# Kernel optimization log

Measured on AMD Instinct MI355X. Metric: run time of the kernel, lower is better.

The kernel has to match this reference:

```python
import jax, jax.numpy as jnp
import numpy as np
import itertools

N = 65536          # points
R = 1.0 / 16.0     # radius (forward uses 1/16)
K = 64             # max_num_neighbors in forward call
G = 16             # grid cells per axis (cell size == R)


def _radius_knn_edges(pts):
    """Grid-hashed radius search; per point keep nearest K within R (self-loop included),
    pad with self index so every point has exactly K edges (max-aggregation neutral)."""
    cells = np.minimum((pts / R).astype(np.int64), G - 1)
    cid = (cells[:, 0] * G + cells[:, 1]) * G + cells[:, 2]
    order = np.argsort(cid, kind='stable')
    sorted_cid = cid[order]
    counts = np.bincount(cid, minlength=G ** 3)
    starts = np.concatenate([[0], np.cumsum(counts)[:-1]])
    M = int(counts.max())
    cand = -np.ones((G ** 3, M), dtype=np.int64)
    slot = np.arange(N) - starts[sorted_cid]
    cand[sorted_cid, slot] = order
    offs = np.array(list(itertools.product([-1, 0, 1], repeat=3)))
    nbr = np.empty((N, K), dtype=np.int64)
    chunk = 4096
    for s in range(0, N, chunk):
        e = min(s + chunk, N)
        c = cells[s:e]
        nc = c[:, None, :] + offs[None]                      # [B,27,3]
        valid_c = np.all((nc >= 0) & (nc < G), axis=-1)      # [B,27]
        ncid = (nc[..., 0] * G + nc[..., 1]) * G + nc[..., 2]
        ncid = np.where(valid_c, ncid, 0)
        cd = cand[ncid]                                      # [B,27,M]
        cd = np.where(np.broadcast_to(valid_c[..., None], cd.shape), cd, -1)
        cd = cd.reshape(e - s, -1)                           # [B,27M]
        p = pts[np.maximum(cd, 0)]
        d = np.linalg.norm(p - pts[s:e, None, :], axis=-1)
        d = np.where((cd >= 0) & (d <= R), d, np.inf)
        sel = np.argsort(d, axis=1)[:, :K]
        row = np.arange(e - s)[:, None]
        picked = cd[row, sel]
        ok = np.isfinite(d[row, sel])
        nbr[s:e] = np.where(ok, picked, np.arange(s, e)[:, None])
    out_index = np.repeat(np.arange(N, dtype=np.int64), K)
    in_index = nbr.reshape(-1)
    return out_index, in_index


def setup_inputs() -> dict:
    key = jax.random.key(0)
    ks = jax.random.split(key, 16)
    pos = jax.random.uniform(ks[0], (N, 3), dtype=jnp.float32)
    rgb = jax.random.uniform(ks[1], (N, 3), dtype=jnp.float32)
    batch = jnp.zeros((N,), dtype=jnp.int64)
    oi, ii = _radius_knn_edges(np.asarray(pos, dtype=np.float64))
    out_index = jnp.asarray(oi)
    in_index = jnp.asarray(ii)

    def lin_w(k, fi, fo):
        return jax.random.normal(k, (fi, fo), dtype=jnp.float32) / np.sqrt(fi).astype(np.float32)

    def lin_b(k, fo):
        return 0.01 * jax.random.normal(k, (fo,), dtype=jnp.float32)

    return {
        'pos': pos, 'rgb': rgb, 'batch': batch,
        'out_index': out_index, 'in_index': in_index,
        'w1a': lin_w(ks[2], 6, 8),   'b1a': lin_b(ks[3], 8),
        'w1b': lin_w(ks[4], 8, 8),   'b1b': lin_b(ks[5], 8),
        'w2a': lin_w(ks[6], 11, 16), 'b2a': lin_b(ks[7], 16),
        'w2b': lin_w(ks[8], 16, 16), 'b2b': lin_b(ks[9], 16),
        'w3a': lin_w(ks[10], 19, 32), 'b3a': lin_b(ks[11], 32),
        'w3b': lin_w(ks[12], 32, 32), 'b3b': lin_b(ks[13], 32),
    }


def _point_conv(x, pos, out_index, in_index, wa, ba, wb, bb):
    # gather neighbor features + relative position, local MLP, max-scatter, output linear
    dpos = pos[in_index] - pos[out_index]                      # [E,3]
    msg = jnp.concatenate([x[in_index], dpos], axis=-1)        # [E,c_in+3]
    h = jax.nn.celu(msg @ wa + ba)                             # [E,c_mid]
    agg = jax.ops.segment_max(h, out_index, num_segments=pos.shape[0],
                              indices_are_sorted=True)         # [N,c_mid]
    return agg @ wb + bb                                       # [N,c_out]


def reference(pos, rgb, batch, out_index, in_index,
              w1a, b1a, w1b, b1b, w2a, b2a, w2b, b2b, w3a, b3a, w3b, b3b):
    out = jax.nn.celu(_point_conv(pos, pos, out_index, in_index, w1a, b1a, w1b, b1b))
    out = jax.nn.celu(_point_conv(out, pos, out_index, in_index, w2a, b2a, w2b, b2b))
    out = jax.nn.celu(_point_conv(out, pos, out_index, in_index, w3a, b3a, w3b, b3b))
    return (pos, out, batch)
```

## Files before the change

### kernel.cpp

```cpp
#include <hip/hip_runtime.h>
#include <hip/hip_fp16.h>
#include <math.h>


#define NPTS 65536
#define KNBR 64

__device__ __forceinline__ float celu1(float x) {
    return x > 0.0f ? x : (__expf(x) - 1.0f);
}

__device__ __forceinline__ unsigned pkmax(unsigned a, unsigned b) {
    unsigned d;
    asm("v_pk_max_f16 %0, %1, %2" : "=v"(d) : "v"(a), "v"(b));
    return d;
}

__device__ __forceinline__ unsigned pack2(float a, float b) {
    __half2 h = __floats2half2_rn(a, b);
    return *(unsigned*)&h;
}

__global__ __launch_bounds__(256) void k_prep1(
    const float* __restrict__ pos,
    const float* __restrict__ w1a,
    const float* __restrict__ b1a,
    __half* __restrict__ q1,
    float* __restrict__ dout,
    int out_size)
{
    int t = blockIdx.x * 256 + threadIdx.x;
    if (t >= NPTS) return;
    float p0 = pos[3 * t + 0];
    float p1 = pos[3 * t + 1];
    float p2 = pos[3 * t + 2];
    dout[3 * t + 0] = p0;
    dout[3 * t + 1] = p1;
    dout[3 * t + 2] = p2;
    float q[8];
#pragma unroll
    for (int c = 0; c < 8; ++c) {
        float a = b1a[c];
        a = fmaf(p0, w1a[0 * 8 + c] + w1a[3 * 8 + c], a);
        a = fmaf(p1, w1a[1 * 8 + c] + w1a[4 * 8 + c], a);
        a = fmaf(p2, w1a[2 * 8 + c] + w1a[5 * 8 + c], a);
        q[c] = a;
    }
    uint4 pk;
    pk.x = pack2(q[0], q[1]);
    pk.y = pack2(q[2], q[3]);
    pk.z = pack2(q[4], q[5]);
    pk.w = pack2(q[6], q[7]);
    *(uint4*)(q1 + 8 * t) = pk;
    for (int j = 35 * NPTS + t; j < out_size; j += NPTS)
        dout[j] = 0.0f;
}

template <int FH>
__global__ __launch_bounds__(256) void k_edge(
    const __half* __restrict__ q,
    const int* __restrict__ idx,
    __half* __restrict__ m)
{
    constexpr int SL  = FH / 8;
    constexpr int EG  = 16 / SL;
    constexpr int EPG = 64 / EG;

    int wave = (blockIdx.x * 256 + threadIdx.x) >> 6;
    int l  = threadIdx.x & 63;
    int pl = l >> 4;
    int u  = l & 15;
    int c  = u % SL;
    int g  = u / SL;
    int p  = wave * 4 + pl;

    const uint4* ip = (const uint4*)(idx + p * KNBR + g * EPG);
    uint4 iv[EPG / 4];
#pragma unroll
    for (int k = 0; k < EPG / 4; ++k) iv[k] = ip[k];

    unsigned ax = 0xFC00FC00u, ay = 0xFC00FC00u, az = 0xFC00FC00u, aw = 0xFC00FC00u;
#pragma unroll
    for (int k = 0; k < EPG / 4; ++k) {
        int j0 = (int)iv[k].x, j1 = (int)iv[k].y, j2 = (int)iv[k].z, j3 = (int)iv[k].w;
        uint4 v0 = *(const uint4*)(q + j0 * FH + c * 8);
        uint4 v1 = *(const uint4*)(q + j1 * FH + c * 8);
        uint4 v2 = *(const uint4*)(q + j2 * FH + c * 8);
        uint4 v3 = *(const uint4*)(q + j3 * FH + c * 8);
        ax = pkmax(ax, v0.x); ay = pkmax(ay, v0.y); az = pkmax(az, v0.z); aw = pkmax(aw, v0.w);
        ax = pkmax(ax, v1.x); ay = pkmax(ay, v1.y); az = pkmax(az, v1.z); aw = pkmax(aw, v1.w);
        ax = pkmax(ax, v2.x); ay = pkmax(ay, v2.y); az = pkmax(az, v2.z); aw = pkmax(aw, v2.w);
        ax = pkmax(ax, v3.x); ay = pkmax(ay, v3.y); az = pkmax(az, v3.z); aw = pkmax(aw, v3.w);
    }
#pragma unroll
    for (int st = SL; st < 16; st <<= 1) {
        ax = pkmax(ax, (unsigned)__shfl_xor((int)ax, st, 64));
        ay = pkmax(ay, (unsigned)__shfl_xor((int)ay, st, 64));
        az = pkmax(az, (unsigned)__shfl_xor((int)az, st, 64));
        aw = pkmax(aw, (unsigned)__shfl_xor((int)aw, st, 64));
    }
    if (g == 0) {
        uint4 r; r.x = ax; r.y = ay; r.z = az; r.w = aw;
        *(uint4*)(m + p * FH + c * 8) = r;
    }
}

template <int FH, int FOUT, int FHN, bool WRITEX>
__global__ __launch_bounds__(256) void k_finish(
    const __half* __restrict__ m,
    const float* __restrict__ pos,
    const float* __restrict__ wap,
    const float* __restrict__ wb,
    const float* __restrict__ bb,
    const float* __restrict__ wan,
    const float* __restrict__ ban,
    float* __restrict__ xout,
    __half* __restrict__ qnext)
{
    int t = blockIdx.x * 256 + threadIdx.x;
    float p0 = pos[3 * t + 0];
    float p1 = pos[3 * t + 1];
    float p2 = pos[3 * t + 2];

    float h[FH];
    const uint4* mr = (const uint4*)(m + t * FH);
#pragma unroll
    for (int l = 0; l < FH / 8; ++l) {
        uint4 v = mr[l];
        unsigned w4[4] = {v.x, v.y, v.z, v.w};
#pragma unroll
        for (int k = 0; k < 4; ++k) {
            float2 f = __half22float2(*(__half2*)&w4[k]);
            h[l * 8 + k * 2 + 0] = f.x;
            h[l * 8 + k * 2 + 1] = f.y;
        }
    }
#pragma unroll
    for (int c = 0; c < FH; ++c) {
        float g = p0 * wap[c] + p1 * wap[FH + c] + p2 * wap[2 * FH + c];
        h[c] = celu1(h[c] - g);
    }
    float x[FOUT];
#pragma unroll
    for (int c2 = 0; c2 < FOUT; ++c2) {
        float a = bb[c2];
#pragma unroll
        for (int c = 0; c < FH; ++c)
            a = fmaf(h[c], wb[c * FOUT + c2], a);
        x[c2] = celu1(a);
    }
    if constexpr (WRITEX) {
        float4* xo = (float4*)(xout + t * FOUT);
#pragma unroll
        for (int c4 = 0; c4 < FOUT / 4; ++c4)
            xo[c4] = make_float4(x[4 * c4 + 0], x[4 * c4 + 1], x[4 * c4 + 2], x[4 * c4 + 3]);
    }
    if constexpr (FHN > 0) {
        float qn[FHN];
#pragma unroll
        for (int cn = 0; cn < FHN; ++cn) {
            float a = ban[cn];
#pragma unroll
            for (int c2 = 0; c2 < FOUT; ++c2)
                a = fmaf(x[c2], wan[c2 * FHN + cn], a);
            a = fmaf(p0, wan[(FOUT + 0) * FHN + cn], a);
            a = fmaf(p1, wan[(FOUT + 1) * FHN + cn], a);
            a = fmaf(p2, wan[(FOUT + 2) * FHN + cn], a);
            qn[cn] = a;
        }
        uint4* qo = (uint4*)(qnext + t * FHN);
#pragma unroll
        for (int l = 0; l < FHN / 8; ++l) {
            uint4 pk;
            pk.x = pack2(qn[l * 8 + 0], qn[l * 8 + 1]);
            pk.y = pack2(qn[l * 8 + 2], qn[l * 8 + 3]);
            pk.z = pack2(qn[l * 8 + 4], qn[l * 8 + 5]);
            pk.w = pack2(qn[l * 8 + 6], qn[l * 8 + 7]);
            qo[l] = pk;
        }
    }
}

extern "C" void kernel_launch(void* const* d_in, const int* in_sizes, int n_in,
                              void* d_out, int out_size, void* d_ws, size_t ws_size,
                              hipStream_t stream) {
    const float* pos = (const float*)d_in[0];
    const int* idx = (const int*)d_in[4];
    const float* w1a = (const float*)d_in[5];
    const float* b1a = (const float*)d_in[6];
    const float* w1b = (const float*)d_in[7];
    const float* b1b = (const float*)d_in[8];
    const float* w2a = (const float*)d_in[9];
    const float* b2a = (const float*)d_in[10];
    const float* w2b = (const float*)d_in[11];
    const float* b2b = (const float*)d_in[12];
    const float* w3a = (const float*)d_in[13];
    const float* b3a = (const float*)d_in[14];
    const float* w3b = (const float*)d_in[15];
    const float* b3b = (const float*)d_in[16];
    float* out = (float*)d_out;

    char* ws = (char*)d_ws;
    __half* A = (__half*)ws;
    __half* B = (__half*)(ws + 8u * 1024u * 1024u);

    k_prep1<<<NPTS / 256, 256, 0, stream>>>(pos, w1a, b1a, A, out, out_size);
    k_edge<8><<<NPTS / 16, 256, 0, stream>>>(A, idx, B);
    k_finish<8, 8, 16, false><<<NPTS / 256, 256, 0, stream>>>(
        B, pos, w1a + 3 * 8, w1b, b1b, w2a, b2a, nullptr, A);
    k_edge<16><<<NPTS / 16, 256, 0, stream>>>(A, idx, B);
    k_finish<16, 16, 32, false><<<NPTS / 256, 256, 0, stream>>>(
        B, pos, w2a + 8 * 16, w2b, b2b, w3a, b3a, nullptr, A);
    k_edge<32><<<NPTS / 16, 256, 0, stream>>>(A, idx, B);
    k_finish<32, 32, 0, true><<<NPTS / 256, 256, 0, stream>>>(
        B, pos, w3a + 16 * 32, w3b, b3b, nullptr, nullptr, out + 3 * NPTS, nullptr);
}
```

Measured before the change: 193.9 us.

## Reorder points by spatial grid cell to improve gather locality

Adds on-device counting-sort of points by grid cell (histogram, scan, slot assignment) and remaps the neighbor index table into sorted order, so every edge gather reads features of spatially nearby points stored contiguously. The final output is scattered back to the original order via a permutation. This targets cache misses in the three random-gather edge kernels but adds five extra launches, atomics and a full index remap pass every call.

```diff
diff --git a/kernel.cpp b/kernel.cpp
--- a/kernel.cpp
+++ b/kernel.cpp
@@ -5,6 +5,8 @@
 
 #define NPTS 65536
 #define KNBR 64
+#define GRES 16
+#define NCELL 4096
 
 __device__ __forceinline__ float celu1(float x) {
     return x > 0.0f ? x : (__expf(x) - 1.0f);
@@ -21,13 +23,63 @@
     return *(unsigned*)&h;
 }
 
-__global__ __launch_bounds__(256) void k_prep1(
+__device__ __forceinline__ int cell_of(float p0, float p1, float p2) {
+    int cx = min((int)(p0 * 16.0f), 15);
+    int cy = min((int)(p1 * 16.0f), 15);
+    int cz = min((int)(p2 * 16.0f), 15);
+    return (cx * GRES + cy) * GRES + cz;
+}
+
+
+__global__ __launch_bounds__(256) void k_zero(int* __restrict__ buf) {
+    buf[blockIdx.x * 256 + threadIdx.x] = 0;
+}
+
+__global__ __launch_bounds__(256) void k_hist(
+    const float* __restrict__ pos, int* __restrict__ counts)
+{
+    int t = blockIdx.x * 256 + threadIdx.x;
+    if (t >= NPTS) return;
+    int cid = cell_of(pos[3 * t], pos[3 * t + 1], pos[3 * t + 2]);
+    atomicAdd(&counts[cid], 1);
+}
+
+__global__ void k_scan(const int* __restrict__ counts, int* __restrict__ starts) {
+    int lane = threadIdx.x;
+    const int4* cp = (const int4*)counts;
+    int4 c[16];
+#pragma unroll
+    for (int k = 0; k < 16; ++k) c[k] = cp[lane * 16 + k];
+    int T = 0;
+#pragma unroll
+    for (int k = 0; k < 16; ++k) T += c[k].x + c[k].y + c[k].z + c[k].w;
+    int inc = T;
+#pragma unroll
+    for (int d = 1; d < 64; d <<= 1) {
+        int u = __shfl_up(inc, d, 64);
+        if (lane >= d) inc += u;
+    }
+    int run = inc - T;
+    int4* sp = (int4*)starts;
+#pragma unroll
+    for (int k = 0; k < 16; ++k) {
+        int4 v = c[k], o;
+        o.x = run; run += v.x;
+        o.y = run; run += v.y;
+        o.z = run; run += v.z;
+        o.w = run; run += v.w;
+        sp[lane * 16 + k] = o;
+    }
+}
+
+__global__ __launch_bounds__(256) void k_slot(
     const float* __restrict__ pos,
-    const float* __restrict__ w1a,
-    const float* __restrict__ b1a,
+    const int* __restrict__ starts, int* __restrict__ cursor,
+    int* __restrict__ slot_of, int* __restrict__ perm,
+    float* __restrict__ pos_s,
+    const float* __restrict__ w1a, const float* __restrict__ b1a,
     __half* __restrict__ q1,
-    float* __restrict__ dout,
-    int out_size)
+    float* __restrict__ dout, int out_size)
 {
     int t = blockIdx.x * 256 + threadIdx.x;
     if (t >= NPTS) return;
@@ -37,6 +89,17 @@
     dout[3 * t + 0] = p0;
     dout[3 * t + 1] = p1;
     dout[3 * t + 2] = p2;
+    for (int j = 35 * NPTS + t; j < out_size; j += NPTS)
+        dout[j] = 0.0f;
+
+    int cid = cell_of(p0, p1, p2);
+    int s = starts[cid] + atomicAdd(&cursor[cid], 1);
+    slot_of[t] = s;
+    perm[s] = t;
+    pos_s[3 * s + 0] = p0;
+    pos_s[3 * s + 1] = p1;
+    pos_s[3 * s + 2] = p2;
+
     float q[8];
 #pragma unroll
     for (int c = 0; c < 8; ++c) {
@@ -51,9 +114,20 @@
     pk.y = pack2(q[2], q[3]);
     pk.z = pack2(q[4], q[5]);
     pk.w = pack2(q[6], q[7]);
-    *(uint4*)(q1 + 8 * t) = pk;
-    for (int j = 35 * NPTS + t; j < out_size; j += NPTS)
-        dout[j] = 0.0f;
+    *(uint4*)(q1 + 8 * s) = pk;
+}
+
+__global__ __launch_bounds__(256) void k_remap(
+    const int* __restrict__ idx,
+    const int* __restrict__ perm,
+    const int* __restrict__ slot_of,
+    int* __restrict__ idxs)
+{
+    int w = (blockIdx.x * 256 + threadIdx.x) >> 6;
+    int k = threadIdx.x & 63;
+    int src = perm[w];
+    int j = idx[src * 64 + k];
+    idxs[w * 64 + k] = slot_of[j];
 }
 
 template <int FH>
@@ -108,19 +182,20 @@
 template <int FH, int FOUT, int FHN, bool WRITEX>
 __global__ __launch_bounds__(256) void k_finish(
     const __half* __restrict__ m,
-    const float* __restrict__ pos,
+    const float* __restrict__ pos_s,
     const float* __restrict__ wap,
     const float* __restrict__ wb,
     const float* __restrict__ bb,
     const float* __restrict__ wan,
     const float* __restrict__ ban,
+    const int* __restrict__ perm,
     float* __restrict__ xout,
     __half* __restrict__ qnext)
 {
     int t = blockIdx.x * 256 + threadIdx.x;
-    float p0 = pos[3 * t + 0];
-    float p1 = pos[3 * t + 1];
-    float p2 = pos[3 * t + 2];
+    float p0 = pos_s[3 * t + 0];
+    float p1 = pos_s[3 * t + 1];
+    float p2 = pos_s[3 * t + 2];
 
     float h[FH];
     const uint4* mr = (const uint4*)(m + t * FH);
@@ -150,7 +225,8 @@
         x[c2] = celu1(a);
     }
     if constexpr (WRITEX) {
-        float4* xo = (float4*)(xout + t * FOUT);
+        int orig = perm[t];
+        float4* xo = (float4*)(xout + (long long)orig * FOUT);
 #pragma unroll
         for (int c4 = 0; c4 < FOUT / 4; ++c4)
             xo[c4] = make_float4(x[4 * c4 + 0], x[4 * c4 + 1], x[4 * c4 + 2], x[4 * c4 + 3]);
@@ -201,17 +277,30 @@
     float* out = (float*)d_out;
 
     char* ws = (char*)d_ws;
-    __half* A = (__half*)ws;
-    __half* B = (__half*)(ws + 8u * 1024u * 1024u);
-
-    k_prep1<<<NPTS / 256, 256, 0, stream>>>(pos, w1a, b1a, A, out, out_size);
-    k_edge<8><<<NPTS / 16, 256, 0, stream>>>(A, idx, B);
+    int*    idxs    = (int*)ws;
+    __half* A       = (__half*)(ws + (16u << 20));
+    __half* B       = (__half*)(ws + (20u << 20));
+    float*  pos_s   = (float*)(ws + (24u << 20));
+    int*    slot_of = (int*)(ws + (25u << 20));
+    int*    perm    = (int*)(ws + (25u << 20) + (256u << 10));
+    int*    counts  = (int*)(ws + (26u << 20));
+    int*    cursor  = counts + NCELL;
+    int*    starts  = cursor + NCELL;
+
+    k_zero<<<2 * NCELL / 256, 256, 0, stream>>>(counts);
+    k_hist<<<NPTS / 256, 256, 0, stream>>>(pos, counts);
+    k_scan<<<1, 64, 0, stream>>>(counts, starts);
+    k_slot<<<NPTS / 256, 256, 0, stream>>>(pos, starts, cursor, slot_of, perm,
+                                           pos_s, w1a, b1a, A, out, out_size);
+    k_remap<<<NPTS / 4, 256, 0, stream>>>(idx, perm, slot_of, idxs);
+
+    k_edge<8><<<NPTS / 16, 256, 0, stream>>>(A, idxs, B);
     k_finish<8, 8, 16, false><<<NPTS / 256, 256, 0, stream>>>(
-        B, pos, w1a + 3 * 8, w1b, b1b, w2a, b2a, nullptr, A);
-    k_edge<16><<<NPTS / 16, 256, 0, stream>>>(A, idx, B);
+        B, pos_s, w1a + 3 * 8, w1b, b1b, w2a, b2a, perm, nullptr, A);
+    k_edge<16><<<NPTS / 16, 256, 0, stream>>>(A, idxs, B);
     k_finish<16, 16, 32, false><<<NPTS / 256, 256, 0, stream>>>(
-        B, pos, w2a + 8 * 16, w2b, b2b, w3a, b3a, nullptr, A);
-    k_edge<32><<<NPTS / 16, 256, 0, stream>>>(A, idx, B);
+        B, pos_s, w2a + 8 * 16, w2b, b2b, w3a, b3a, perm, nullptr, A);
+    k_edge<32><<<NPTS / 16, 256, 0, stream>>>(A, idxs, B);
     k_finish<32, 32, 0, true><<<NPTS / 256, 256, 0, stream>>>(
-        B, pos, w3a + 16 * 32, w3b, b3b, nullptr, nullptr, out + 3 * NPTS, nullptr);
-}
+        B, pos_s, w3a + 16 * 32, w3b, b3b, nullptr, nullptr, perm, out + 3 * NPTS, nullptr);
+}
```

Result: slower. 199.3 us (+2.8%).

## Fuse edge max-gather and per-point finish into one kernel per layer

Applied to the files above, without the earlier changes.

Merges the gather/max-aggregation kernel and the per-point MLP finish kernel into a single kernel per layer. Aggregated maxima for 64 points stay in shared memory instead of being written to and reread from global memory. This removes three launches and a global round trip per layer. The cost is a block barrier, and only one wave of each block runs the finish step, which idles the other three and may lower occupancy.

```diff
diff --git a/kernel.cpp b/kernel.cpp
--- a/kernel.cpp
+++ b/kernel.cpp
@@ -21,7 +21,7 @@
     return *(unsigned*)&h;
 }
 
-__global__ __launch_bounds__(256) void k_prep1(
+__global__ __launch_bounds__(256) void k_prep(
     const float* __restrict__ pos,
     const float* __restrict__ w1a,
     const float* __restrict__ b1a,
@@ -56,58 +56,10 @@
         dout[j] = 0.0f;
 }
 
-template <int FH>
-__global__ __launch_bounds__(256) void k_edge(
+template <int FH, int FOUT, int FHN, bool WRITEX>
+__global__ __launch_bounds__(256) void k_layer(
     const __half* __restrict__ q,
     const int* __restrict__ idx,
-    __half* __restrict__ m)
-{
-    constexpr int SL  = FH / 8;
-    constexpr int EG  = 16 / SL;
-    constexpr int EPG = 64 / EG;
-
-    int wave = (blockIdx.x * 256 + threadIdx.x) >> 6;
-    int l  = threadIdx.x & 63;
-    int pl = l >> 4;
-    int u  = l & 15;
-    int c  = u % SL;
-    int g  = u / SL;
-    int p  = wave * 4 + pl;
-
-    const uint4* ip = (const uint4*)(idx + p * KNBR + g * EPG);
-    uint4 iv[EPG / 4];
-#pragma unroll
-    for (int k = 0; k < EPG / 4; ++k) iv[k] = ip[k];
-
-    unsigned ax = 0xFC00FC00u, ay = 0xFC00FC00u, az = 0xFC00FC00u, aw = 0xFC00FC00u;
-#pragma unroll
-    for (int k = 0; k < EPG / 4; ++k) {
-        int j0 = (int)iv[k].x, j1 = (int)iv[k].y, j2 = (int)iv[k].z, j3 = (int)iv[k].w;
-        uint4 v0 = *(const uint4*)(q + j0 * FH + c * 8);
-        uint4 v1 = *(const uint4*)(q + j1 * FH + c * 8);
-        uint4 v2 = *(const uint4*)(q + j2 * FH + c * 8);
-        uint4 v3 = *(const uint4*)(q + j3 * FH + c * 8);
-        ax = pkmax(ax, v0.x); ay = pkmax(ay, v0.y); az = pkmax(az, v0.z); aw = pkmax(aw, v0.w);
-        ax = pkmax(ax, v1.x); ay = pkmax(ay, v1.y); az = pkmax(az, v1.z); aw = pkmax(aw, v1.w);
-        ax = pkmax(ax, v2.x); ay = pkmax(ay, v2.y); az = pkmax(az, v2.z); aw = pkmax(aw, v2.w);
-        ax = pkmax(ax, v3.x); ay = pkmax(ay, v3.y); az = pkmax(az, v3.z); aw = pkmax(aw, v3.w);
-    }
-#pragma unroll
-    for (int st = SL; st < 16; st <<= 1) {
-        ax = pkmax(ax, (unsigned)__shfl_xor((int)ax, st, 64));
-        ay = pkmax(ay, (unsigned)__shfl_xor((int)ay, st, 64));
-        az = pkmax(az, (unsigned)__shfl_xor((int)az, st, 64));
-        aw = pkmax(aw, (unsigned)__shfl_xor((int)aw, st, 64));
-    }
-    if (g == 0) {
-        uint4 r; r.x = ax; r.y = ay; r.z = az; r.w = aw;
-        *(uint4*)(m + p * FH + c * 8) = r;
-    }
-}
-
-template <int FH, int FOUT, int FHN, bool WRITEX>
-__global__ __launch_bounds__(256) void k_finish(
-    const __half* __restrict__ m,
     const float* __restrict__ pos,
     const float* __restrict__ wap,
     const float* __restrict__ wb,
@@ -117,66 +69,122 @@
     float* __restrict__ xout,
     __half* __restrict__ qnext)
 {
-    int t = blockIdx.x * 256 + threadIdx.x;
-    float p0 = pos[3 * t + 0];
-    float p1 = pos[3 * t + 1];
-    float p2 = pos[3 * t + 2];
-
-    float h[FH];
-    const uint4* mr = (const uint4*)(m + t * FH);
-#pragma unroll
-    for (int l = 0; l < FH / 8; ++l) {
-        uint4 v = mr[l];
-        unsigned w4[4] = {v.x, v.y, v.z, v.w};
-#pragma unroll
-        for (int k = 0; k < 4; ++k) {
-            float2 f = __half22float2(*(__half2*)&w4[k]);
-            h[l * 8 + k * 2 + 0] = f.x;
-            h[l * 8 + k * 2 + 1] = f.y;
+    constexpr int SL  = FH / 8;
+    constexpr int LPP = SL * 8;
+    constexpr int PPW = 64 / LPP;
+    constexpr int NIT = 64 / (4 * PPW);
+
+    __shared__ uint4 m_lds[64 * SL];
+
+    int w  = threadIdx.x >> 6;
+    int l  = threadIdx.x & 63;
+    int pl = l / LPP;
+    int u  = l % LPP;
+    int c  = u % SL;
+    int g  = u / SL;
+    int pbase = blockIdx.x * 64;
+
+#pragma unroll
+    for (int it = 0; it < NIT; ++it) {
+        int lp = it * (4 * PPW) + w * PPW + pl;
+        int p  = pbase + lp;
+        const uint4* ip = (const uint4*)(idx + p * KNBR + g * 8);
+        uint4 i0 = ip[0];
+        uint4 i1 = ip[1];
+        uint4 v[8];
+        v[0] = *(const uint4*)(q + (int)i0.x * FH + c * 8);
+        v[1] = *(const uint4*)(q + (int)i0.y * FH + c * 8);
+        v[2] = *(const uint4*)(q + (int)i0.z * FH + c * 8);
+        v[3] = *(const uint4*)(q + (int)i0.w * FH + c * 8);
+        v[4] = *(const uint4*)(q + (int)i1.x * FH + c * 8);
+        v[5] = *(const uint4*)(q + (int)i1.y * FH + c * 8);
+        v[6] = *(const uint4*)(q + (int)i1.z * FH + c * 8);
+        v[7] = *(const uint4*)(q + (int)i1.w * FH + c * 8);
+
+        unsigned ax = 0xFC00FC00u, ay = 0xFC00FC00u, az = 0xFC00FC00u, aw = 0xFC00FC00u;
+#pragma unroll
+        for (int k = 0; k < 8; ++k) {
+            ax = pkmax(ax, v[k].x);
+            ay = pkmax(ay, v[k].y);
+            az = pkmax(az, v[k].z);
+            aw = pkmax(aw, v[k].w);
+        }
+#pragma unroll
+        for (int st = SL; st < LPP; st <<= 1) {
+            ax = pkmax(ax, (unsigned)__shfl_xor((int)ax, st, 64));
+            ay = pkmax(ay, (unsigned)__shfl_xor((int)ay, st, 64));
+            az = pkmax(az, (unsigned)__shfl_xor((int)az, st, 64));
+            aw = pkmax(aw, (unsigned)__shfl_xor((int)aw, st, 64));
+        }
+        if (g == 0) {
+            uint4 r; r.x = ax; r.y = ay; r.z = az; r.w = aw;
+            m_lds[lp * SL + c] = r;
         }
     }
-#pragma unroll
-    for (int c = 0; c < FH; ++c) {
-        float g = p0 * wap[c] + p1 * wap[FH + c] + p2 * wap[2 * FH + c];
-        h[c] = celu1(h[c] - g);
-    }
-    float x[FOUT];
-#pragma unroll
-    for (int c2 = 0; c2 < FOUT; ++c2) {
-        float a = bb[c2];
-#pragma unroll
-        for (int c = 0; c < FH; ++c)
-            a = fmaf(h[c], wb[c * FOUT + c2], a);
-        x[c2] = celu1(a);
-    }
-    if constexpr (WRITEX) {
-        float4* xo = (float4*)(xout + t * FOUT);
-#pragma unroll
-        for (int c4 = 0; c4 < FOUT / 4; ++c4)
-            xo[c4] = make_float4(x[4 * c4 + 0], x[4 * c4 + 1], x[4 * c4 + 2], x[4 * c4 + 3]);
-    }
-    if constexpr (FHN > 0) {
-        float qn[FHN];
-#pragma unroll
-        for (int cn = 0; cn < FHN; ++cn) {
-            float a = ban[cn];
-#pragma unroll
-            for (int c2 = 0; c2 < FOUT; ++c2)
-                a = fmaf(x[c2], wan[c2 * FHN + cn], a);
-            a = fmaf(p0, wan[(FOUT + 0) * FHN + cn], a);
-            a = fmaf(p1, wan[(FOUT + 1) * FHN + cn], a);
-            a = fmaf(p2, wan[(FOUT + 2) * FHN + cn], a);
-            qn[cn] = a;
-        }
-        uint4* qo = (uint4*)(qnext + t * FHN);
-#pragma unroll
-        for (int l = 0; l < FHN / 8; ++l) {
-            uint4 pk;
-            pk.x = pack2(qn[l * 8 + 0], qn[l * 8 + 1]);
-            pk.y = pack2(qn[l * 8 + 2], qn[l * 8 + 3]);
-            pk.z = pack2(qn[l * 8 + 4], qn[l * 8 + 5]);
-            pk.w = pack2(qn[l * 8 + 6], qn[l * 8 + 7]);
-            qo[l] = pk;
+    __syncthreads();
+
+    if (threadIdx.x < 64) {
+        int lt = threadIdx.x;
+        int p  = pbase + lt;
+        float p0 = pos[3 * p + 0];
+        float p1 = pos[3 * p + 1];
+        float p2 = pos[3 * p + 2];
+
+        float h[FH];
+#pragma unroll
+        for (int s = 0; s < SL; ++s) {
+            uint4 vv = m_lds[lt * SL + s];
+            unsigned w4[4] = {vv.x, vv.y, vv.z, vv.w};
+#pragma unroll
+            for (int k = 0; k < 4; ++k) {
+                float2 f = __half22float2(*(__half2*)&w4[k]);
+                h[s * 8 + k * 2 + 0] = f.x;
+                h[s * 8 + k * 2 + 1] = f.y;
+            }
+        }
+#pragma unroll
+        for (int ch = 0; ch < FH; ++ch) {
+            float gg = p0 * wap[ch] + p1 * wap[FH + ch] + p2 * wap[2 * FH + ch];
+            h[ch] = celu1(h[ch] - gg);
+        }
+        float x[FOUT];
+#pragma unroll
+        for (int c2 = 0; c2 < FOUT; ++c2) {
+            float a = bb[c2];
+#pragma unroll
+            for (int ch = 0; ch < FH; ++ch)
+                a = fmaf(h[ch], wb[ch * FOUT + c2], a);
+            x[c2] = celu1(a);
+        }
+        if constexpr (WRITEX) {
+            float4* xo = (float4*)(xout + (long long)p * FOUT);
+#pragma unroll
+            for (int c4 = 0; c4 < FOUT / 4; ++c4)
+                xo[c4] = make_float4(x[4 * c4 + 0], x[4 * c4 + 1], x[4 * c4 + 2], x[4 * c4 + 3]);
+        }
+        if constexpr (FHN > 0) {
+            float qn[FHN];
+#pragma unroll
+            for (int cn = 0; cn < FHN; ++cn) {
+                float a = ban[cn];
+#pragma unroll
+                for (int c2 = 0; c2 < FOUT; ++c2)
+                    a = fmaf(x[c2], wan[c2 * FHN + cn], a);
+                a = fmaf(p0, wan[(FOUT + 0) * FHN + cn], a);
+                a = fmaf(p1, wan[(FOUT + 1) * FHN + cn], a);
+                a = fmaf(p2, wan[(FOUT + 2) * FHN + cn], a);
+                qn[cn] = a;
+            }
+            uint4* qo = (uint4*)(qnext + p * FHN);
+#pragma unroll
+            for (int s = 0; s < FHN / 8; ++s) {
+                uint4 pk;
+                pk.x = pack2(qn[s * 8 + 0], qn[s * 8 + 1]);
+                pk.y = pack2(qn[s * 8 + 2], qn[s * 8 + 3]);
+                pk.z = pack2(qn[s * 8 + 4], qn[s * 8 + 5]);
+                pk.w = pack2(qn[s * 8 + 6], qn[s * 8 + 7]);
+                qo[s] = pk;
+            }
         }
     }
 }
@@ -202,16 +210,13 @@
 
     char* ws = (char*)d_ws;
     __half* A = (__half*)ws;
-    __half* B = (__half*)(ws + 8u * 1024u * 1024u);
-
-    k_prep1<<<NPTS / 256, 256, 0, stream>>>(pos, w1a, b1a, A, out, out_size);
-    k_edge<8><<<NPTS / 16, 256, 0, stream>>>(A, idx, B);
-    k_finish<8, 8, 16, false><<<NPTS / 256, 256, 0, stream>>>(
-        B, pos, w1a + 3 * 8, w1b, b1b, w2a, b2a, nullptr, A);
-    k_edge<16><<<NPTS / 16, 256, 0, stream>>>(A, idx, B);
-    k_finish<16, 16, 32, false><<<NPTS / 256, 256, 0, stream>>>(
-        B, pos, w2a + 8 * 16, w2b, b2b, w3a, b3a, nullptr, A);
-    k_edge<32><<<NPTS / 16, 256, 0, stream>>>(A, idx, B);
-    k_finish<32, 32, 0, true><<<NPTS / 256, 256, 0, stream>>>(
-        B, pos, w3a + 16 * 32, w3b, b3b, nullptr, nullptr, out + 3 * NPTS, nullptr);
-}
+    __half* B = (__half*)(ws + (4u << 20));
+
+    k_prep<<<NPTS / 256, 256, 0, stream>>>(pos, w1a, b1a, A, out, out_size);
+    k_layer<8, 8, 16, false><<<NPTS / 64, 256, 0, stream>>>(
+        A, idx, pos, w1a + 3 * 8, w1b, b1b, w2a, b2a, nullptr, B);
+    k_layer<16, 16, 32, false><<<NPTS / 64, 256, 0, stream>>>(
+        B, idx, pos, w2a + 8 * 16, w2b, b2b, w3a, b3a, nullptr, A);
+    k_layer<32, 32, 0, true><<<NPTS / 64, 256, 0, stream>>>(
+        A, idx, pos, w3a + 16 * 32, w3b, b3b, nullptr, nullptr, out + 3 * NPTS, nullptr);
+}
```

Measured after the change: 179.1 us. -7.6%, faster.
